# Kernel optimization log

Measured on AMD Instinct MI355X. Metric: run time of the kernel, lower is better.

## Reference

```python
import jax, jax.numpy as jnp
import numpy as np

SR = 16000; NFFT = 1024; HOP = 256; NMELS = 80; GRUH = 256; ZDIM = 16
NBINS = 65; HID = 512; B = 8; TLEN = 160000; PAD = NFFT // 2; IRLEN = 8000

def _consts():
    freqs = np.linspace(0, SR / 2, NFFT // 2 + 1); fsq = freqs ** 2
    aw = (12194.217 ** 2 * fsq ** 2) / ((fsq + 20.6 ** 2) * (fsq + 107.7 ** 2) * (fsq + 737.9 ** 2) * (fsq + 12194.217 ** 2) ** 0.5 + 1e-8)
    h2m = lambda f: 2595.0 * np.log10(1.0 + f / 700.0)
    m2h = lambda m: 700.0 * (10.0 ** (m / 2595.0) - 1.0)
    f_pts = m2h(np.linspace(h2m(0.0), h2m(SR / 2.0), NMELS + 2))
    fd = f_pts[1:] - f_pts[:-1]
    sl = f_pts[None, :] - freqs[:, None]
    fb = np.maximum(0.0, np.minimum(-sl[:, :-2] / fd[:-1], sl[:, 2:] / fd[1:]))
    win = 0.5 - 0.5 * np.cos(2.0 * np.pi * np.arange(NFFT) / NFFT)  # periodic hann
    return jnp.asarray(aw, jnp.float32), jnp.asarray(fb, jnp.float32), jnp.asarray(win, jnp.float32)
AW, MELFB, WIN = _consts()

def _frame(x, size, hop):
    n = (x.shape[-1] - size) // hop + 1
    idx = jnp.arange(n)[:, None] * hop + jnp.arange(size)[None, :]
    return x[:, idx]

def _stft(x):  # [B,T] -> [B, n_frames, 513] complex
    xp = jnp.pad(x, ((0, 0), (PAD, PAD)), mode='reflect')
    return jnp.fft.rfft(_frame(xp, NFFT, HOP) * WIN, axis=-1)

def _istft(spec, length):  # [B, n_frames, 513] -> [B, length]
    fr = jnp.fft.irfft(spec, n=NFFT, axis=-1) * WIN
    n = fr.shape[1]; total = (n - 1) * HOP + NFFT
    idx = (jnp.arange(n)[:, None] * HOP + jnp.arange(NFFT)[None, :]).reshape(-1)
    out = jnp.zeros((fr.shape[0], total), fr.dtype).at[:, idx].add(fr.reshape(fr.shape[0], -1))
    wsq = jnp.zeros((total,), WIN.dtype).at[idx].add(jnp.tile(WIN ** 2, (n,)))
    out = out / jnp.where(wsq > 1e-11, wsq, 1.0)
    return out[:, PAD:PAD + length]

def _lin_interp(x, size):  # torch F.interpolate(mode='linear', align_corners=False) on last axis
    L = x.shape[-1]
    pos = jnp.clip((jnp.arange(size) + 0.5) * (L / size) - 0.5, 0.0, L - 1.0)
    lo = jnp.floor(pos).astype(jnp.int32); hi = jnp.minimum(lo + 1, L - 1); w = pos - lo
    return x[..., lo] * (1.0 - w) + x[..., hi] * w

def _gru(x, wih, whh, bih, bhh):  # torch nn.GRU, batch_first, h0=0
    xp = x @ wih.T + bih
    def step(h, xt):
        gh = h @ whh.T + bhh
        xr, xz, xn = jnp.split(xt, 3, -1); hr, hz, hn = jnp.split(gh, 3, -1)
        r = jax.nn.sigmoid(xr + hr); z = jax.nn.sigmoid(xz + hz)
        nn_ = jnp.tanh(xn + r * hn)
        h = (1.0 - z) * nn_ + z * h
        return h, h
    h0 = jnp.zeros((x.shape[0], whh.shape[1]), x.dtype)
    _, hs = jax.lax.scan(step, h0, jnp.swapaxes(xp, 0, 1))
    return jnp.swapaxes(hs, 0, 1)

def _forward(audio, gender, age, gru_wih, gru_whh, gru_bih, gru_bhh, proj_w, proj_b,
             w0, b0, g0, e0, w1, b1, g1, e1, w2, b2, g2, e2,
             oq_w, oq_b, vt_w, vt_b, nf_w, nf_b, ir):
    # --- pitch via autocorrelation ---
    xp = jnp.pad(audio, ((0, 0), (PAD, PAD)), mode='reflect')
    fr = _frame(xp, NFFT, HOP)
    ps = jnp.abs(jnp.fft.rfft(fr, n=2 * NFFT, axis=-1)) ** 2
    ac = jnp.fft.irfft(ps, n=2 * NFFT, axis=-1)[..., :NFFT]
    ac = ac / (ac[..., :1] + 1e-8)
    min_lag, max_lag = SR // 1000, SR // 50  # 16, 320
    reg = ac[..., min_lag:max_lag]
    mv = jnp.max(reg, -1); mi = jnp.argmax(reg, -1)
    f0 = SR / (mi.astype(jnp.float32) + min_lag + 1e-8)
    f0 = jnp.where(mv < 0.3, 0.0, f0)[..., None]  # [B,F,1]
    # --- loudness + mels ---
    spec = jnp.abs(_stft(audio)) ** 2  # [B,F,513]
    loud = 10.0 * jnp.log10(jnp.mean((spec + 1e-8) * AW, -1, keepdims=True))  # [B,F,1]
    mels = jnp.log(spec @ MELFB + 1e-5)  # [B,F,80]
    mels = (mels - mels.mean(1, keepdims=True)) / jnp.sqrt(mels.var(1, keepdims=True) + 1e-5)
    z = _gru(mels, gru_wih, gru_whh, gru_bih, gru_bhh) @ proj_w.T + proj_b  # [B,F,16]
    Fn = f0.shape[1]
    # --- controller ---
    gb = jnp.broadcast_to(gender[:, None, :], (gender.shape[0], Fn, 2))
    ab = jnp.broadcast_to(age[:, None, :], (age.shape[0], Fn, 1))
    h = jnp.concatenate([z, (jnp.log(f0 + 1e-5) - 4.0) / 4.0, loud / 100.0 + 1.0, gb, ab], -1)
    for W, bb, gm, bt in ((w0, b0, g0, e0), (w1, b1, g1, e1), (w2, b2, g2, e2)):
        h = h @ W.T + bb
        h = (h - h.mean(-1, keepdims=True)) / jnp.sqrt(h.var(-1, keepdims=True) + 1e-5) * gm + bt
        h = jnp.where(h >= 0, h, 0.1 * h)  # LeakyReLU(0.1)
    oq = jax.nn.sigmoid(h @ oq_w.T + oq_b)
    vt = jax.nn.sigmoid(h @ vt_w.T + vt_b)
    nf = jax.nn.sigmoid(h @ nf_w.T + nf_b)
    amp = 10.0 ** (loud / 20.0)
    # --- decoder ---
    L = audio.shape[-1]
    f0u = _lin_interp(f0[..., 0], L); ampu = _lin_interp(amp[..., 0], L); oqu = _lin_interp(oq[..., 0], L)
    phase = jnp.cumsum(f0u / SR, -1); p = phase - jnp.floor(phase)
    oqc = jnp.clip(oqu, 0.1, 0.9)
    pulse = 0.5 * (1.0 - jnp.cos(jnp.pi * p / (oqc + 1e-8)))
    g = pulse * jax.nn.sigmoid((oqc - p) * 100.0)
    glottal = jnp.pad(g[..., 1:] - g[..., :-1], ((0, 0), (1, 0)))
    noise = jax.random.normal(jax.random.key(42), glottal.shape, glottal.dtype)
    def apply_filter(ex, filt):
        es = _stft(ex)  # [B,nf,513]
        ft = _lin_interp(jnp.swapaxes(filt, 1, 2), es.shape[1])  # time interp
        ff = _lin_interp(jnp.swapaxes(ft, 1, 2), es.shape[2])    # bin interp 65->513
        return _istft(es * ff, L)
    dry = (apply_filter(glottal, vt) + apply_filter(noise, nf)) * ampu
    # --- FFT reverb ---
    nconv = int(2 ** int(np.ceil(np.log2(L + IRLEN - 1))))
    wet = jnp.fft.irfft(jnp.fft.rfft(dry, n=nconv) * jnp.fft.rfft(ir, n=nconv), n=nconv)[..., :L]
    return wet, dry

def setup_inputs() -> dict:
    ks = iter(jax.random.split(jax.random.key(0), 48))
    def nrm(shape, s=0.05):
        return jax.random.normal(next(ks), shape, jnp.float32) * s
    inp = {}
    inp['audio'] = jax.random.normal(next(ks), (B, TLEN), jnp.float32)
    inp['gender'] = jax.random.uniform(next(ks), (B, 2), jnp.float32)
    inp['age'] = jax.random.uniform(next(ks), (B, 1), jnp.float32)
    inp['gru_wih'] = nrm((3 * GRUH, NMELS)); inp['gru_whh'] = nrm((3 * GRUH, GRUH))
    inp['gru_bih'] = jnp.zeros((3 * GRUH,), jnp.float32); inp['gru_bhh'] = jnp.zeros((3 * GRUH,), jnp.float32)
    inp['proj_w'] = nrm((ZDIM, GRUH)); inp['proj_b'] = jnp.zeros((ZDIM,), jnp.float32)
    din = ZDIM + 5
    inp['w0'] = nrm((HID, din)); inp['b0'] = jnp.zeros((HID,), jnp.float32)
    inp['g0'] = jnp.ones((HID,), jnp.float32); inp['e0'] = jnp.zeros((HID,), jnp.float32)
    inp['w1'] = nrm((HID, HID)); inp['b1'] = jnp.zeros((HID,), jnp.float32)
    inp['g1'] = jnp.ones((HID,), jnp.float32); inp['e1'] = jnp.zeros((HID,), jnp.float32)
    inp['w2'] = nrm((HID, HID)); inp['b2'] = jnp.zeros((HID,), jnp.float32)
    inp['g2'] = jnp.ones((HID,), jnp.float32); inp['e2'] = jnp.zeros((HID,), jnp.float32)
    inp['oq_w'] = nrm((1, HID)); inp['oq_b'] = jnp.zeros((1,), jnp.float32)
    inp['vt_w'] = nrm((NBINS, HID)); inp['vt_b'] = jnp.zeros((NBINS,), jnp.float32)
    inp['nf_w'] = nrm((NBINS, HID)); inp['nf_b'] = jnp.zeros((NBINS,), jnp.float32)
    decay = jnp.exp(-jnp.linspace(0.0, 5.0, IRLEN))
    inp['ir'] = jax.random.normal(next(ks), (IRLEN,), jnp.float32) * 0.1 * decay
    return inp

def reference(audio, gender, age, gru_wih, gru_whh, gru_bih, gru_bhh, proj_w, proj_b,
              w0, b0, g0, e0, w1, b1, g1, e1, w2, b2, g2, e2,
              oq_w, oq_b, vt_w, vt_b, nf_w, nf_b, ir):
    return _forward(audio, gender, age, gru_wih, gru_whh, gru_bih, gru_bhh, proj_w, proj_b,
                    w0, b0, g0, e0, w1, b1, g1, e1, w2, b2, g2, e2,
                    oq_w, oq_b, vt_w, vt_b, nf_w, nf_b, ir)
```

## Files before the change

### kernel.cpp

```cpp
#include <hip/hip_runtime.h>
#include <math.h>

#define SRF 16000.0f
#define HOP 256
#define FRM 626
#define BB 8
#define TLEN 160000
#define NFRM (BB*FRM)
#define NCONV 262144
#define ACCLEN 161024
#define GCH 40

constexpr size_t oWIN   = 0;
constexpr size_t oTW    = oWIN + 1024;
constexpr size_t oDIAG  = oTW + 1024;
constexpr size_t oTWF   = oDIAG + 16;
constexpr size_t oTWC   = oTWF + 1024;
constexpr size_t oAW    = oTWC + 1024;
constexpr size_t oMELFB = oAW + 513;
constexpr size_t oWSQI  = oMELFB + 513*80;
constexpr size_t oWIHT  = oWSQI + ACCLEN;
constexpr size_t oW0T   = oWIHT + 80*768;
constexpr size_t oW1T   = oW0T + 21*512;
constexpr size_t oW2T   = oW1T + 512*512;
constexpr size_t oVTT   = oW2T + 512*512;
constexpr size_t oNFT   = oVTT + 512*65;
constexpr size_t oF0    = oNFT + 512*65;
constexpr size_t oLOUD  = oF0 + NFRM;
constexpr size_t oOQ    = oLOUD + NFRM;
constexpr size_t oVT    = oOQ + NFRM;
constexpr size_t oNF    = oVT + (size_t)NFRM*65;
constexpr size_t oGLOT  = oNF + (size_t)NFRM*65;
constexpr size_t oNOISE = oGLOT + (size_t)BB*TLEN;
constexpr size_t oACC   = oNOISE + (size_t)BB*TLEN;
constexpr size_t oCONVA = oACC + (size_t)BB*ACCLEN;
constexpr size_t oEND   = oCONVA + (size_t)9*NCONV*2;
constexpr size_t oXP    = oEND;
constexpr size_t oGSUM  = oXP + (size_t)NFRM*768;
constexpr size_t oGPRE  = oGSUM + 320;
constexpr size_t oEND2  = oGPRE + 640;
constexpr size_t oCONVB = oWSQI;
constexpr size_t oMEL = oCONVA;
constexpr size_t oHS  = oMEL + (size_t)NFRM*80;

constexpr long R_WIN=1024, R_TW=512, R_TWF=512, R_TWC=512, R_AW=513, R_MELFB=41040,
  R_WSQI=161024, R_WIHT=61440, R_W0T=10752, R_W1T=262144, R_W2T=262144,
  R_VTT=33280, R_NFT=33280, R_IR=NCONV;
constexpr long INIT_TOTAL = R_WIN+R_TW+R_TWF+R_TWC+R_AW+R_MELFB+R_WSQI+R_WIHT+R_W0T+
  R_W1T+R_W2T+R_VTT+R_NFT+R_IR;

constexpr int NOISEB = 313;
constexpr int ZACCB  = 315;
constexpr int MEGA_BLOCKS = 1 + NFRM + NOISEB + ZACCB;

typedef float f32x4 __attribute__((ext_vector_type(4)));
typedef __bf16 bf16x8 __attribute__((ext_vector_type(8)));
typedef short short8 __attribute__((ext_vector_type(8)));
#define MFMA_BF16 __builtin_amdgcn_mfma_f32_16x16x32_bf16

__device__ inline int mirror_idx(int j) {
  if (j < 0) j = -j;
  if (j >= TLEN) j = 2*TLEN - 2 - j;
  return j;
}
__device__ inline float sigm(float x) { return 1.0f/(1.0f + expf(-x)); }
__device__ inline unsigned short f2bf(float x) {
  unsigned u = __float_as_uint(x);
  return (unsigned short)((u + 0x7FFFu + ((u >> 16) & 1u)) >> 16);
}
__device__ inline float tanh_fast(float x) {
  return 1.0f - 2.0f/(__expf(2.0f*x) + 1.0f);
}

__device__ inline float interpF(const float* v, int i) {
  float pos = ((float)i + 0.5f) * (626.0f/160000.0f) - 0.5f;
  pos = fminf(fmaxf(pos, 0.0f), 625.0f);
  int lo = (int)floorf(pos);
  int hi = min(lo + 1, 625);
  float w = pos - (float)lo;
  return v[lo]*(1.0f - w) + v[hi]*w;
}
__device__ inline float interp65(const float* v, int k) {
  float pos = ((float)k + 0.5f) * (65.0f/513.0f) - 0.5f;
  pos = fminf(fmaxf(pos, 0.0f), 64.0f);
  int lo = (int)floorf(pos);
  int hi = min(lo + 1, 64);
  float w = pos - (float)lo;
  return v[lo]*(1.0f - w) + v[hi]*w;
}
__device__ inline float gwave(float ph, float oqu) {
  float p = ph - floorf(ph);
  float oqc = fminf(fmaxf(oqu, 0.1f), 0.9f);
  float pulse = 0.5f*(1.0f - cosf(3.14159265358979f * p / (oqc + 1e-8f)));
  float gs = 1.0f/(1.0f + __expf(-(oqc - p)*100.0f));
  return pulse*gs;
}

template<int LOGN, int TS>
__device__ inline void fft2(float2* c, const float2* tw, int tid, int nthr, bool inv) {
  constexpr int N = 1 << LOGN;
  for (int s = 1; s <= LOGN; ++s) {
    const int half = 1 << (s-1);
    const int tstep = (N >> s) * TS;
    for (int bf = tid; bf < (N>>1); bf += nthr) {
      int jj = bf & (half-1);
      int i0 = ((bf >> (s-1)) << s) + jj;
      int i1 = i0 + half;
      float2 wv = tw[jj*tstep];
      float wi = inv ? -wv.y : wv.y;
      float2 u = c[i0], v = c[i1];
      float tr  = v.x*wv.x - v.y*wi;
      float tci = v.x*wi  + v.y*wv.x;
      c[i0] = make_float2(u.x + tr, u.y + tci);
      c[i1] = make_float2(u.x - tr, u.y - tci);
    }
    __syncthreads();
  }
}

__device__ inline void threefry2x32(unsigned k0, unsigned k1, unsigned x0, unsigned x1,
                                    unsigned& o0, unsigned& o1) {
  unsigned ks2 = k0 ^ k1 ^ 0x1BD11BDAu;
  x0 += k0; x1 += k1;
#define TF_R(r) { x0 += x1; x1 = (x1<<(r)) | (x1>>(32-(r))); x1 ^= x0; }
  TF_R(13) TF_R(15) TF_R(26) TF_R(6)
  x0 += k1; x1 += ks2 + 1u;
  TF_R(17) TF_R(29) TF_R(16) TF_R(24)
  x0 += ks2; x1 += k0 + 2u;
  TF_R(13) TF_R(15) TF_R(26) TF_R(6)
  x0 += k0; x1 += k1 + 3u;
  TF_R(17) TF_R(29) TF_R(16) TF_R(24)
  x0 += k1; x1 += ks2 + 4u;
  TF_R(13) TF_R(15) TF_R(26) TF_R(6)
  x0 += ks2; x1 += k0 + 5u;
#undef TF_R
  o0 = x0; o1 = x1;
}

__device__ inline float erfinv_f(float x) {
  float w = -log1pf(-x*x);
  float p;
  if (w < 5.0f) {
    w = w - 2.5f;
    p = 2.81022636e-08f;
    p = fmaf(p, w, 3.43273939e-07f);
    p = fmaf(p, w, -3.5233877e-06f);
    p = fmaf(p, w, -4.39150654e-06f);
    p = fmaf(p, w, 0.00021858087f);
    p = fmaf(p, w, -0.00125372503f);
    p = fmaf(p, w, -0.00417768164f);
    p = fmaf(p, w, 0.246640727f);
    p = fmaf(p, w, 1.50140941f);
  } else {
    w = sqrtf(w) - 3.0f;
    p = -0.000200214257f;
    p = fmaf(p, w, 0.000100950558f);
    p = fmaf(p, w, 0.00134934322f);
    p = fmaf(p, w, -0.00367342844f);
    p = fmaf(p, w, 0.00573950773f);
    p = fmaf(p, w, -0.0076224613f);
    p = fmaf(p, w, 0.00943887047f);
    p = fmaf(p, w, 1.00167406f);
    p = fmaf(p, w, 2.83297682f);
  }
  return p*x;
}
__device__ inline float normal_from_bits(unsigned bits) {
  float f = __uint_as_float((bits >> 9) | 0x3F800000u) - 1.0f;
  float x = fmaxf(-0.99999994f, fmaf(f, 1.99999994f, -0.99999994f));
  return 1.41421356237f * erfinv_f(x);
}

__device__ inline double mel_fpt(int j) {
  double mmax = 2595.0 * log10(1.0 + 8000.0/700.0);
  return 700.0 * (pow(10.0, (mmax * (double)j / 81.0) / 2595.0) - 1.0);
}

__global__ void k_init(float* W, const float* wih, const float* w0,
                       const float* w1, const float* w2, const float* vtw, const float* nfw,
                       const float* ir) {
  long id = (long)blockIdx.x*256 + threadIdx.x;
  if (id < R_WIN) {
    double w = 0.5 - 0.5*cos(2.0*M_PI*(double)id/1024.0);
    W[oWIN+id] = (float)w; return;
  } id -= R_WIN;
  if (id < R_TW) {
    double a = -2.0*M_PI*(double)id/1024.0;
    W[oTW+2*id] = (float)cos(a); W[oTW+2*id+1] = (float)sin(a); return;
  } id -= R_TW;
  if (id < R_TWF) {
    double a = -2.0*M_PI*(double)id/262144.0;
    W[oTWF+2*id] = (float)cos(a); W[oTWF+2*id+1] = (float)sin(a); return;
  } id -= R_TWF;
  if (id < R_TWC) {
    double a = -2.0*M_PI*(double)id/512.0;
    W[oTWC+2*id] = (float)cos(a); W[oTWC+2*id+1] = (float)sin(a); return;
  } id -= R_TWC;
  if (id < R_AW) {
    double fr = (double)id*(8000.0/512.0); double fsq = fr*fr;
    double num = 12194.217*12194.217*fsq*fsq;
    double den = (fsq+20.6*20.6)*(fsq+107.7*107.7)*(fsq+737.9*737.9)*sqrt(fsq+12194.217*12194.217) + 1e-8;
    W[oAW+id] = (float)(num/den); return;
  } id -= R_AW;
  if (id < R_MELFB) {
    int k = (int)(id/80), m = (int)(id%80);
    double fk = (double)k*(8000.0/512.0);
    double f0p = mel_fpt(m), f1p = mel_fpt(m+1), f2p = mel_fpt(m+2);
    double lower = (fk - f0p)/(f1p - f0p);
    double upper = (f2p - fk)/(f2p - f1p);
    double v = fmax(0.0, fmin(lower, upper));
    W[oMELFB+id] = (float)v; return;
  } id -= R_MELFB;
  if (id < R_WSQI) {
    int t = (int)id;
    int n1 = t/256; if (n1 > 625) n1 = 625;
    int n0t = t - 1023 + 255; int n0 = (n0t > 0) ? n0t/256 : 0;
    double s = 0.0;
    for (int n = n0; n <= n1; ++n) {
      int o = t - n*256;
      double wv = 0.5 - 0.5*cos(2.0*M_PI*(double)o/1024.0);
      s += wv*wv;
    }
    float sf = (float)s;
    W[oWSQI+t] = (sf > 1e-11f) ? (1.0f/sf) : 1.0f; return;
  } id -= R_WSQI;
  if (id < R_WIHT) { long k = id/768, g = id%768; W[oWIHT+id] = wih[g*80+k];  return; } id -= R_WIHT;
  if (id < R_W0T)  { long d = id/512, j = id%512; W[oW0T+id] = w0[j*21+d];   return; } id -= R_W0T;
  if (id < R_W1T)  { long k = id/512, j = id%512; W[oW1T+id] = w1[j*512+k];  return; } id -= R_W1T;
  if (id < R_W2T)  { long k = id/512, j = id%512; W[oW2T+id] = w2[j*512+k];  return; } id -= R_W2T;
  if (id < R_VTT)  { long k = id/65,  m = id%65;  W[oVTT+id] = vtw[m*512+k]; return; } id -= R_VTT;
  if (id < R_NFT)  { long k = id/65,  m = id%65;  W[oNFT+id] = nfw[m*512+k]; return; } id -= R_NFT;
  if (id < R_IR) {
    size_t base = oCONVA + 2*((size_t)8*NCONV + id);
    W[base] = (id < 8000) ? ir[id] : 0.0f; W[base+1] = 0.0f; return;
  }
}

__global__ __launch_bounds__(256) void k_stft_mel(const float* audio, float* W) {
  int blk = blockIdx.x; int b = blk/FRM, f = blk%FRM; int tid = threadIdx.x;
  __shared__ float2 cb[1024];
  __shared__ float spec[513];
  __shared__ float redbuf[4];
  const float* arow = audio + (size_t)b*TLEN;
  const float2* tw = (const float2*)(W + oTW);
  for (int i = tid; i < 1024; i += 256) {
    float v = arow[mirror_idx(f*256 + i - 512)] * W[oWIN + i];
    int pos = __brev((unsigned)i) >> 22;
    cb[pos] = make_float2(v, 0.f);
  }
  __syncthreads();
  fft2<10,1>(cb, tw, tid, 256, false);
  for (int k = tid; k < 513; k += 256) { float2 z = cb[k]; spec[k] = z.x*z.x + z.y*z.y; }
  __syncthreads();
  float part = 0.f;
  for (int k = tid; k < 513; k += 256) part += (spec[k] + 1e-8f) * W[oAW + k];
  for (int off = 32; off; off >>= 1) part += __shfl_down(part, off, 64);
  if ((tid & 63) == 0) redbuf[tid >> 6] = part;
  __syncthreads();
  if (tid == 0) {
    float s = redbuf[0]+redbuf[1]+redbuf[2]+redbuf[3];
    W[oLOUD + blk] = 10.0f * log10f(s / 513.0f);
  }
  for (int m = tid; m < 80; m += 256) {
    double f0p = mel_fpt(m), f2p = mel_fpt(m + 2);
    int klo = (int)(f0p * (512.0/8000.0)); if (klo < 0) klo = 0;
    int khi = (int)(f2p * (512.0/8000.0)) + 1; if (khi > 512) khi = 512;
    float s = 0.f;
    for (int k = klo; k <= khi; ++k) s += spec[k]*W[oMELFB + (size_t)k*80 + m];
    W[oMEL + (size_t)blk*80 + m] = logf(s + 1e-5f);
  }
}

__global__ void k_melnorm(float* W) {
  int id = blockIdx.x*256 + threadIdx.x;
  if (id >= BB*80) return;
  int b = id/80, m = id%80;
  double s = 0.0, ss = 0.0;
  for (int f = 0; f < FRM; ++f) {
    double v = W[oMEL + ((size_t)b*FRM + f)*80 + m];
    s += v; ss += v*v;
  }
  double mean = s/FRM;
  double var = ss/FRM - mean*mean;
  float mu = (float)mean;
  float rstd = (float)(1.0/sqrt(var + 1e-5));
  for (int f = 0; f < FRM; ++f) {
    size_t idx = oMEL + ((size_t)b*FRM + f)*80 + m;
    W[idx] = (W[idx] - mu)*rstd;
  }
}

__global__ void k_xp(float* W, const float* bih) {
  size_t id = (size_t)blockIdx.x*256 + threadIdx.x;
  if (id >= (size_t)NFRM*768) return;
  int g = (int)(id % 768);
  size_t q = id / 768;
  const float* mrow = W + oMEL + q*80;
  float acc = bih[g];
  for (int k = 0; k < 80; ++k) acc = fmaf(mrow[k], W[oWIHT + (size_t)k*768 + g], acc);
  W[oXP + q*768 + g] = acc;
}

__global__ __launch_bounds__(512, 2) void k_mega(float* W, const float* audio,
                                                 const float* whh, const float* bhh) {
  __shared__ unsigned short sB[32768];
  __shared__ unsigned short sA[4096];
  __shared__ float sGT[9216];
  __shared__ float fr4[4][1032];
  __shared__ float wpow[8];
  __shared__ float wmax[8];
  __shared__ int   wmaxi[8];
  int tid = threadIdx.x;
  int blk = blockIdx.x;

  if (blk == 0) {
    int w = tid >> 6, l = tid & 63;
    const float* XP = W + oXP;
    float* HS = W + oHS;

    for (int idx = tid; idx < 32768; idx += 512) {
      int lcol = idx >> 8, k = idx & 255;
      int gcol = 96*(lcol >> 4) + 80 + (lcol & 15);
      sB[lcol*256 + (k ^ ((lcol & 7) << 3))] = f2bf(whh[(size_t)gcol*256 + k]);
    }
    for (int idx = tid; idx < 4096; idx += 512) sA[idx] = 0;

    int cl = l & 15, khalf = (l >> 4) * 8;
    bf16x8 bw[40];
    #pragma unroll
    for (int t2 = 0; t2 < 5; ++t2) {
      int col = 96*w + 16*t2 + cl;
      #pragma unroll
      for (int kk = 0; kk < 8; ++kk) {
        const float* src = whh + (size_t)col*256 + kk*32 + khalf;
        short8 tmp;
        #pragma unroll
        for (int j = 0; j < 8; ++j) tmp[j] = (short)f2bf(src[j]);
        bw[t2*8 + kk] = __builtin_bit_cast(bf16x8, tmp);
      }
    }

    int g = tid & 255, bbase = tid >> 8;
    float bh_r = bhh[g], bh_z = bhh[256 + g], bh_n = bhh[512 + g];
    float hprev[4] = {0.f, 0.f, 0.f, 0.f};
    int aXor = (cl & 7) << 3;
    int lcol5 = w*16 + cl;
    int rowg = l >> 4;
    int colb = 96*w + cl;
    int gtw = colb*12 + rowg*4;
    int gtr0 = g*12 + 4*bbase;
    int gtr1 = (256 + g)*12 + 4*bbase;
    int gtr2 = (512 + g)*12 + 4*bbase;

    __syncthreads();

#define LDA(kk) (*(const bf16x8*)&sA[(cl)*256 + (((kk)*32 + khalf) ^ aXor)])
#define LDB(kk) (*(const bf16x8*)&sB[(lcol5)*256 + (((kk)*32 + khalf) ^ aXor)])
#define STEPK(A_, kk) \
      c0 = MFMA_BF16(A_, bw[0*8+(kk)], c0, 0, 0, 0); \
      c1 = MFMA_BF16(A_, bw[1*8+(kk)], c1, 0, 0, 0); \
      c2 = MFMA_BF16(A_, bw[2*8+(kk)], c2, 0, 0, 0); \
      c3 = MFMA_BF16(A_, bw[3*8+(kk)], c3, 0, 0, 0); \
      c4 = MFMA_BF16(A_, bw[4*8+(kk)], c4, 0, 0, 0); \
      c5 = MFMA_BF16(A_, LDB(kk), c5, 0, 0, 0);

    for (int t = 0; t < FRM; ++t) {
      float xr[4], xz[4], xn[4];
      #pragma unroll
      for (int j = 0; j < 4; ++j) {
        const float* xpp = XP + ((size_t)(4*bbase + j)*FRM + t)*768 + g;
        xr[j] = xpp[0]; xz[j] = xpp[256]; xn[j] = xpp[512];
      }
      f32x4 c0 = {0,0,0,0}, c1 = {0,0,0,0}, c2 = {0,0,0,0};
      f32x4 c3 = {0,0,0,0}, c4 = {0,0,0,0}, c5 = {0,0,0,0};
      bf16x8 a0 = LDA(0), a1 = LDA(1), a2 = LDA(2), a3 = LDA(3);
      STEPK(a0, 0) STEPK(a1, 1) STEPK(a2, 2) STEPK(a3, 3)
      a0 = LDA(4); a1 = LDA(5); a2 = LDA(6); a3 = LDA(7);
      STEPK(a0, 4) STEPK(a1, 5) STEPK(a2, 6) STEPK(a3, 7)
      if (rowg < 3) {
        *(f32x4*)&sGT[gtw + 0*192]  = c0;
        *(f32x4*)&sGT[gtw + 1*192]  = c1;
        *(f32x4*)&sGT[gtw + 2*192]  = c2;
        *(f32x4*)&sGT[gtw + 3*192]  = c3;
        *(f32x4*)&sGT[gtw + 4*192]  = c4;
        *(f32x4*)&sGT[gtw + 5*192]  = c5;
      }
      __syncthreads();
      f32x4 rv = *(const f32x4*)&sGT[gtr0];
      f32x4 zv = *(const f32x4*)&sGT[gtr1];
      f32x4 nv = *(const f32x4*)&sGT[gtr2];
      #pragma unroll
      for (int j = 0; j < 4; ++j) {
        int bb = 4*bbase + j;
        float r = 1.0f/(1.0f + __expf(-(xr[j] + rv[j] + bh_r)));
        float z = 1.0f/(1.0f + __expf(-(xz[j] + zv[j] + bh_z)));
        float nn = tanh_fast(xn[j] + r*(nv[j] + bh_n));
        float h = (1.0f - z)*nn + z*hprev[j];
        hprev[j] = h;
        HS[((size_t)bb*FRM + t)*256 + g] = h;
        sA[bb*256 + (g ^ ((bb & 7) << 3))] = f2bf(h);
      }
      __syncthreads();
    }
#undef LDA
#undef LDB
#undef STEPK
    return;
  }
  blk -= 1;

  if (blk < NFRM) {
    int b = blk/FRM, f = blk%FRM;
    const float* arow = audio + (size_t)b*TLEN;
    for (int idx = tid; idx < 4*1032; idx += 512) {
      int s = idx/1032, i = idx - s*1032;
      int j = i + s;
      fr4[s][i] = (j < 1024) ? arow[mirror_idx(f*256 + j - 512)] : 0.f;
    }
    __syncthreads();
    int lane = tid & 63, wv = tid >> 6;
    float p = 0.f;
    for (int i = tid; i < 1024; i += 512) { float x = fr4[0][i]; p += x*x; }
    for (int off = 32; off; off >>= 1) p += __shfl_down(p, off, 64);
    if (lane == 0) wpow[wv] = p;
    float vbest = -1e30f; int ibest = tid;
    if (tid < 304) {
      int lag = 16 + tid;
      int s = lag & 3, base = lag - s;
      int qmax = (1023 - lag) >> 2;
      float acc = 0.f;
      for (int q = 0; q <= qmax; ++q) {
        float4 u = *(const float4*)&fr4[0][4*q];
        float4 v = *(const float4*)&fr4[s][base + 4*q];
        acc += u.x*v.x + u.y*v.y + u.z*v.z + u.w*v.w;
      }
      vbest = acc;
    }
    for (int off = 32; off; off >>= 1) {
      float v2 = __shfl_down(vbest, off, 64);
      int i2 = __shfl_down(ibest, off, 64);
      if (v2 > vbest || (v2 == vbest && i2 < ibest)) { vbest = v2; ibest = i2; }
    }
    if (lane == 0) { wmax[wv] = vbest; wmaxi[wv] = ibest; }
    __syncthreads();
    if (tid == 0) {
      float ac0 = 0.f;
      #pragma unroll
      for (int q = 0; q < 8; ++q) ac0 += wpow[q];
      float bv = wmax[0]; int bi = wmaxi[0];
      #pragma unroll
      for (int q = 1; q < 8; ++q) {
        if (wmax[q] > bv || (wmax[q] == bv && wmaxi[q] < bi)) { bv = wmax[q]; bi = wmaxi[q]; }
      }
      float inv = 1.0f/(ac0 + 1e-8f);
      float best = bv*inv;
      W[oF0 + (size_t)blk] = (best < 0.3f) ? 0.0f : (SRF/(float)(bi + 16));
    }
    return;
  }
  blk -= NFRM;

  if (blk < NOISEB) {
    size_t base = (size_t)blk*4096;
    #pragma unroll
    for (int j = 0; j < 8; ++j) {
      size_t p = base + (size_t)j*512 + tid;
      if (p < (size_t)BB*TLEN) {
        unsigned o0, o1;
        threefry2x32(0u, 42u, 0u, (unsigned)p, o0, o1);
        W[oNOISE + p] = normal_from_bits(o0 ^ o1);
      }
    }
    return;
  }
  blk -= NOISEB;

  {
    size_t base = (size_t)blk*4096;
    #pragma unroll
    for (int j = 0; j < 8; ++j) {
      size_t p = base + (size_t)j*512 + tid;
      if (p < (size_t)BB*ACCLEN) W[oACC + p] = 0.0f;
    }
  }
}

__device__ inline void ln_lrelu(float acc[8], float gj, float ej, float out[8][512],
                                float wred[8][8][2], float stat[8][2],
                                int tid, int lane, int wv, int j) {
  #pragma unroll
  for (int i = 0; i < 8; ++i) {
    float s = acc[i], ss = acc[i]*acc[i];
    for (int off = 32; off; off >>= 1) { s += __shfl_down(s, off, 64); ss += __shfl_down(ss, off, 64); }
    if (lane == 0) { wred[i][wv][0] = s; wred[i][wv][1] = ss; }
  }
  __syncthreads();
  if (tid < 8) {
    float s = 0.f, ss = 0.f;
    #pragma unroll
    for (int w = 0; w < 8; ++w) { s += wred[tid][w][0]; ss += wred[tid][w][1]; }
    float mean = s/512.0f;
    float var = ss/512.0f - mean*mean;
    stat[tid][0] = mean;
    stat[tid][1] = 1.0f/sqrtf(var + 1e-5f);
  }
  __syncthreads();
  #pragma unroll
  for (int i = 0; i < 8; ++i) {
    float v = (acc[i] - stat[i][0])*stat[i][1]*gj + ej;
    out[i][j] = (v >= 0.f) ? v : 0.1f*v;
  }
}

__global__ __launch_bounds__(512) void k_mlp(float* W, const float* gender, const float* age,
    const float* projw, const float* projb,
    const float* b0, const float* g0, const float* e0,
    const float* b1, const float* g1, const float* e1,
    const float* b2, const float* g2, const float* e2,
    const float* oqw, const float* oqb, const float* vtb, const float* nfb) {
  __shared__ float hbuf[8][256];
  __shared__ float in0[8][21];
  __shared__ float actA[8][512];
  __shared__ float actB[8][512];
  __shared__ float wred[8][8][2];
  __shared__ float stat[8][2];
  int tid = threadIdx.x; int q0 = blockIdx.x*8;
  for (int x = tid; x < 2048; x += 512) {
    int i = x >> 8, k = x & 255;
    hbuf[i][k] = W[oHS + ((size_t)(q0 + i))*256 + k];
  }
  __syncthreads();
  if (tid < 128) {
    int i = tid >> 4, zi = tid & 15;
    float a = projb[zi];
    for (int k = 0; k < 256; ++k) a = fmaf(hbuf[i][k], projw[zi*256 + k], a);
    in0[i][zi] = a;
  } else if (tid < 168) {
    int x = tid - 128; int i = x/5, d = 16 + x%5;
    int q = q0 + i; int b = q/FRM;
    float v;
    if (d == 16) v = (logf(W[oF0 + q] + 1e-5f) - 4.0f)*0.25f;
    else if (d == 17) v = W[oLOUD + q]/100.0f + 1.0f;
    else if (d == 18) v = gender[b*2];
    else if (d == 19) v = gender[b*2 + 1];
    else v = age[b];
    in0[i][d] = v;
  }
  __syncthreads();
  int j = tid, lane = tid & 63, wv = tid >> 6;
  float acc[8];
  #pragma unroll
  for (int i = 0; i < 8; ++i) acc[i] = b0[j];
  for (int d = 0; d < 21; ++d) {
    float w = W[oW0T + (size_t)d*512 + j];
    #pragma unroll
    for (int i = 0; i < 8; ++i) acc[i] = fmaf(in0[i][d], w, acc[i]);
  }
  ln_lrelu(acc, g0[j], e0[j], actA, wred, stat, tid, lane, wv, j);
  __syncthreads();
  #pragma unroll
  for (int i = 0; i < 8; ++i) acc[i] = b1[j];
  for (int k = 0; k < 512; ++k) {
    float w = W[oW1T + (size_t)k*512 + j];
    #pragma unroll
    for (int i = 0; i < 8; ++i) acc[i] = fmaf(actA[i][k], w, acc[i]);
  }
  ln_lrelu(acc, g1[j], e1[j], actB, wred, stat, tid, lane, wv, j);
  __syncthreads();
  #pragma unroll
  for (int i = 0; i < 8; ++i) acc[i] = b2[j];
  for (int k = 0; k < 512; ++k) {
    float w = W[oW2T + (size_t)k*512 + j];
    #pragma unroll
    for (int i = 0; i < 8; ++i) acc[i] = fmaf(actB[i][k], w, acc[i]);
  }
  ln_lrelu(acc, g2[j], e2[j], actA, wred, stat, tid, lane, wv, j);
  __syncthreads();
  for (int x = tid; x < 520; x += 512) {
    int i = x/65, m = x%65;
    float a = vtb[m], a2 = nfb[m];
    for (int k = 0; k < 512; ++k) {
      float h = actA[i][k];
      a  = fmaf(h, W[oVTT + (size_t)k*65 + m], a);
      a2 = fmaf(h, W[oNFT + (size_t)k*65 + m], a2);
    }
    W[oVT + (size_t)(q0+i)*65 + m] = sigm(a);
    W[oNF + (size_t)(q0+i)*65 + m] = sigm(a2);
  }
  if (tid < 8) {
    float a = oqb[0];
    for (int k = 0; k < 512; ++k) a = fmaf(actA[tid][k], oqw[k], a);
    W[oOQ + q0 + tid] = sigm(a);
  }
}

__global__ __launch_bounds__(256) void k_gsum(float* W) {
  int blk = blockIdx.x; int b = blk/GCH, c = blk%GCH; int tid = threadIdx.x;
  __shared__ float ws[4];
  const float* f0r = W + oF0 + (size_t)b*FRM;
  int i0 = c*4096 + tid*16;
  float s = 0.f;
  #pragma unroll
  for (int j = 0; j < 16; ++j) {
    int i = i0 + j;
    if (i < TLEN) s += interpF(f0r, i)*(1.0f/SRF);
  }
  for (int off = 32; off; off >>= 1) s += __shfl_down(s, off, 64);
  if ((tid & 63) == 0) ws[tid >> 6] = s;
  __syncthreads();
  if (tid == 0) W[oGSUM + (size_t)b*GCH + c] = ws[0]+ws[1]+ws[2]+ws[3];
}

__global__ void k_gscan(float* W) {
  if (blockIdx.x == 0 && threadIdx.x == 0) {
    double* P = (double*)(W + oGPRE);
    for (int b = 0; b < BB; ++b) {
      double a = 0.0;
      for (int c = 0; c < GCH; ++c) {
        P[b*GCH + c] = a;
        a += (double)W[oGSUM + (size_t)b*GCH + c];
      }
    }
  }
}

__global__ __launch_bounds__(256) void k_gapply(float* W) {
  int blk = blockIdx.x; int b = blk/GCH, c = blk%GCH; int tid = threadIdx.x;
  __shared__ float wss[4];
  __shared__ float lastw[4];
  const float* f0r = W + oF0 + (size_t)b*FRM;
  const float* oqr = W + oOQ + (size_t)b*FRM;
  float* grow = W + oGLOT + (size_t)b*TLEN;
  double P = ((const double*)(W + oGPRE))[b*GCH + c];
  int i0 = c*4096 + tid*16;
  int lane = tid & 63, wv = tid >> 6;
  float v[16]; float ts = 0.f;
  #pragma unroll
  for (int j = 0; j < 16; ++j) {
    int i = i0 + j;
    float x = (i < TLEN) ? interpF(f0r, i)*(1.0f/SRF) : 0.f;
    v[j] = x; ts += x;
  }
  float sc = ts;
  #pragma unroll
  for (int off = 1; off < 64; off <<= 1) {
    float o = __shfl_up(sc, off, 64);
    if (lane >= off) sc += o;
  }
  if (lane == 63) wss[wv] = sc;
  __syncthreads();
  float wpre = 0.f;
  for (int q = 0; q < wv; ++q) wpre += wss[q];
  double ph0 = P + (double)(wpre + sc - ts);
  float run = 0.f; float gq[16];
  #pragma unroll
  for (int j = 0; j < 16; ++j) {
    int i = i0 + j;
    run += v[j];
    float ph = (float)(ph0 + (double)run);
    gq[j] = gwave(ph, interpF(oqr, min(i, TLEN-1)));
  }
  float prev = __shfl_up(gq[15], 1, 64);
  if (lane == 63) lastw[wv] = gq[15];
  __syncthreads();
  if (lane == 0) {
    if (wv > 0) prev = lastw[wv - 1];
    else if (i0 > 0) prev = gwave((float)P, interpF(oqr, i0 - 1));
    else prev = 0.f;
  }
  #pragma unroll
  for (int j = 0; j < 16; ++j) {
    int i = i0 + j;
    if (i < TLEN) {
      float gl = (j == 0) ? prev : gq[j-1];
      grow[i] = (i == 0) ? 0.f : (gq[j] - gl);
    }
  }
}

__global__ __launch_bounds__(256) void k_filtsynth(float* W) {
  int blk = blockIdx.x; int b = blk/FRM, f = blk%FRM; int tid = threadIdx.x;
  __shared__ float2 cG[1024], cN[1024];
  __shared__ float fvt[65], fnf[65];
  const float* grow = W + oGLOT + (size_t)b*TLEN;
  const float* nrow = W + oNOISE + (size_t)b*TLEN;
  const float2* tw = (const float2*)(W + oTW);
  for (int i = tid; i < 1024; i += 256) {
    int si = mirror_idx(f*256 + i - 512);
    float wv = W[oWIN + i];
    int pos = __brev((unsigned)i) >> 22;
    cG[pos] = make_float2(grow[si]*wv, 0.f);
    cN[pos] = make_float2(nrow[si]*wv, 0.f);
  }
  if (tid < 65) {
    fvt[tid] = W[oVT + ((size_t)b*FRM + f)*65 + tid];
    fnf[tid] = W[oNF + ((size_t)b*FRM + f)*65 + tid];
  }
  __syncthreads();
  fft2<10,1>(cG, tw, tid, 256, false);
  fft2<10,1>(cN, tw, tid, 256, false);
  for (int k = tid; k < 1024; k += 256) {
    int kp = min(k, 1024 - k);
    float fv = interp65(fvt, kp);
    float fn = interp65(fnf, kp);
    float2 zg = cG[k], zn = cN[k];
    cG[k] = make_float2(zg.x*fv + zn.x*fn, zg.y*fv + zn.y*fn);
  }
  __syncthreads();
  for (int i = tid; i < 1024; i += 256) {
    int jj = __brev((unsigned)i) >> 22;
    if (jj > i) { float2 t2 = cG[i]; cG[i] = cG[jj]; cG[jj] = t2; }
  }
  __syncthreads();
  fft2<10,1>(cG, tw, tid, 256, true);
  float* arow = W + oACC + (size_t)b*ACCLEN + (size_t)f*256;
  for (int i = tid; i < 1024; i += 256) {
    float xv = cG[i].x*(1.0f/1024.0f)*W[oWIN + i];
    atomicAdd(arow + i, xv);
  }
}

__global__ void k_dry(float* W, float* dout) {
  size_t id = (size_t)blockIdx.x*256 + threadIdx.x;
  if (id >= (size_t)BB*NCONV) return;
  int b = (int)(id / NCONV);
  int n = (int)(id % NCONV);
  float dv = 0.f;
  if (n < TLEN) {
    float val = W[oACC + (size_t)b*ACCLEN + 512 + n] * W[oWSQI + 512 + n];
    const float* lrow = W + oLOUD + (size_t)b*FRM;
    float pos = ((float)n + 0.5f) * (626.0f/160000.0f) - 0.5f;
    pos = fminf(fmaxf(pos, 0.0f), 625.0f);
    int lo = (int)floorf(pos);
    int hi = min(lo + 1, 625);
    float w = pos - (float)lo;
    float a0 = exp10f(lrow[lo]*0.05f);
    float a1 = exp10f(lrow[hi]*0.05f);
    float ampu = a0*(1.0f - w) + a1*w;
    dv = val*ampu;
    dout[(size_t)BB*TLEN + (size_t)b*TLEN + n] = dv;
  }
  ((float2*)(W + oCONVA))[id] = make_float2(dv, 0.f);
}

__global__ __launch_bounds__(256) void k_conv_f1(const float* in, float* out,
                                                 const float* tw, const float* twf,
                                                 const float* twc) {
  int blk = blockIdx.x; int t = blk >> 9; int bcol = blk & 511; int tid = threadIdx.x;
  __shared__ float2 cb[512];
  const float2* src = (const float2*)in + (size_t)t*NCONV;
  for (int a = tid; a < 512; a += 256) {
    int pos = __brev((unsigned)a) >> 23;
    cb[pos] = src[(size_t)a*512 + bcol];
  }
  __syncthreads();
  fft2<9,2>(cb, (const float2*)tw, tid, 256, false);
  float2* dst = (float2*)out + (size_t)t*NCONV + (size_t)bcol*512;
  for (int k1 = tid; k1 < 512; k1 += 256) {
    unsigned m = (unsigned)bcol * (unsigned)k1;
    float2 tc = ((const float2*)twc)[m >> 9];
    float2 tf = ((const float2*)twf)[m & 511];
    float wr = tc.x*tf.x - tc.y*tf.y;
    float wi = tc.x*tf.y + tc.y*tf.x;
    float2 v = cb[k1];
    dst[k1] = make_float2(v.x*wr - v.y*wi, v.x*wi + v.y*wr);
  }
}

__global__ __launch_bounds__(256) void k_conv_f2(const float* in, float* out, const float* tw) {
  int blk = blockIdx.x; int t = blk >> 9; int k1 = blk & 511; int tid = threadIdx.x;
  __shared__ float2 cb[512];
  const float2* src = (const float2*)in + (size_t)t*NCONV;
  for (int bb2 = tid; bb2 < 512; bb2 += 256) {
    int pos = __brev((unsigned)bb2) >> 23;
    cb[pos] = src[(size_t)bb2*512 + k1];
  }
  __syncthreads();
  fft2<9,2>(cb, (const float2*)tw, tid, 256, false);
  float2* dst = (float2*)out + (size_t)t*NCONV;
  for (int k2 = tid; k2 < 512; k2 += 256) {
    dst[(size_t)k1 + 512*(size_t)k2] = cb[k2];
  }
}

__global__ void k_mul(float* W) {
  size_t id = (size_t)blockIdx.x*256 + threadIdx.x;
  if (id >= (size_t)BB*NCONV) return;
  size_t k = id % NCONV;
  float2* A = (float2*)(W + oCONVA);
  float2 a = A[id];
  float2 c = A[(size_t)8*NCONV + k];
  float pr = a.x*c.x - a.y*c.y;
  float pi = a.x*c.y + a.y*c.x;
  A[id] = make_float2(pr, -pi);
}

__global__ void k_wet(const float* W, float* dout) {
  size_t id = (size_t)blockIdx.x*256 + threadIdx.x;
  if (id >= (size_t)BB*TLEN) return;
  size_t b = id / TLEN, n = id % TLEN;
  dout[id] = ((const float2*)(W + oCONVA))[b*NCONV + n].x * (1.0f/262144.0f);
}

extern "C" void kernel_launch(void* const* d_in, const int* in_sizes, int n_in,
                              void* d_out, int out_size, void* d_ws, size_t ws_size,
                              hipStream_t stream) {
  (void)in_sizes; (void)n_in; (void)out_size; (void)ws_size;
  const float* audio  = (const float*)d_in[0];
  const float* gender = (const float*)d_in[1];
  const float* age    = (const float*)d_in[2];
  const float* wih    = (const float*)d_in[3];
  const float* whh    = (const float*)d_in[4];
  const float* bih    = (const float*)d_in[5];
  const float* bhh    = (const float*)d_in[6];
  const float* projw  = (const float*)d_in[7];
  const float* projb  = (const float*)d_in[8];
  const float* w0     = (const float*)d_in[9];
  const float* b0     = (const float*)d_in[10];
  const float* g0     = (const float*)d_in[11];
  const float* e0     = (const float*)d_in[12];
  const float* w1     = (const float*)d_in[13];
  const float* b1     = (const float*)d_in[14];
  const float* g1     = (const float*)d_in[15];
  const float* e1     = (const float*)d_in[16];
  const float* w2     = (const float*)d_in[17];
  const float* b2     = (const float*)d_in[18];
  const float* g2     = (const float*)d_in[19];
  const float* e2     = (const float*)d_in[20];
  const float* oqw    = (const float*)d_in[21];
  const float* oqb    = (const float*)d_in[22];
  const float* vtw    = (const float*)d_in[23];
  const float* vtb    = (const float*)d_in[24];
  const float* nfw    = (const float*)d_in[25];
  const float* nfb    = (const float*)d_in[26];
  const float* ir     = (const float*)d_in[27];
  float* W = (float*)d_ws;
  float* dout = (float*)d_out;

  k_init<<<(int)((INIT_TOTAL + 255)/256), 256, 0, stream>>>(W, wih, w0, w1, w2, vtw, nfw, ir);
  k_stft_mel<<<NFRM, 256, 0, stream>>>(audio, W);
  k_melnorm<<<3, 256, 0, stream>>>(W);
  k_xp<<<(int)(((size_t)NFRM*768 + 255)/256), 256, 0, stream>>>(W, bih);
  k_mega<<<MEGA_BLOCKS, 512, 0, stream>>>(W, audio, whh, bhh);
  k_mlp<<<NFRM/8, 512, 0, stream>>>(W, gender, age, projw, projb,
                                    b0, g0, e0, b1, g1, e1, b2, g2, e2, oqw, oqb, vtb, nfb);
  k_gsum<<<BB*GCH, 256, 0, stream>>>(W);
  k_gscan<<<1, 64, 0, stream>>>(W);
  k_gapply<<<BB*GCH, 256, 0, stream>>>(W);
  k_filtsynth<<<NFRM, 256, 0, stream>>>(W);
  k_dry<<<(int)(((size_t)BB*NCONV + 255)/256), 256, 0, stream>>>(W, dout);
  k_conv_f1<<<9*512, 256, 0, stream>>>(W + oCONVA, W + oCONVB, W + oTW, W + oTWF, W + oTWC);
  k_conv_f2<<<9*512, 256, 0, stream>>>(W + oCONVB, W + oCONVA, W + oTW);
  k_mul<<<(int)(((size_t)BB*NCONV + 255)/256), 256, 0, stream>>>(W);
  k_conv_f1<<<8*512, 256, 0, stream>>>(W + oCONVA, W + oCONVB, W + oTW, W + oTWF, W + oTWC);
  k_conv_f2<<<8*512, 256, 0, stream>>>(W + oCONVB, W + oCONVA, W + oTW);
  k_wet<<<(int)(((size_t)BB*TLEN + 255)/256), 256, 0, stream>>>(W, dout);
}
```

Measured before the change: 2.229 ms.

## Pack real signals into complex FFTs for filter synthesis and convolution

```diff
diff --git a/kernel.cpp b/kernel.cpp
--- a/kernel.cpp
+++ b/kernel.cpp
@@ -34,7 +34,7 @@
 constexpr size_t oNOISE = oGLOT + (size_t)BB*TLEN;
 constexpr size_t oACC   = oNOISE + (size_t)BB*TLEN;
 constexpr size_t oCONVA = oACC + (size_t)BB*ACCLEN;
-constexpr size_t oEND   = oCONVA + (size_t)9*NCONV*2;
+constexpr size_t oEND   = oCONVA + (size_t)5*NCONV*2;
 constexpr size_t oXP    = oEND;
 constexpr size_t oGSUM  = oXP + (size_t)NFRM*768;
 constexpr size_t oGPRE  = oGSUM + 320;
@@ -231,7 +231,7 @@
   if (id < R_VTT)  { long k = id/65,  m = id%65;  W[oVTT+id] = vtw[m*512+k]; return; } id -= R_VTT;
   if (id < R_NFT)  { long k = id/65,  m = id%65;  W[oNFT+id] = nfw[m*512+k]; return; } id -= R_NFT;
   if (id < R_IR) {
-    size_t base = oCONVA + 2*((size_t)8*NCONV + id);
+    size_t base = oCONVA + 2*((size_t)4*NCONV + id);
     W[base] = (id < 8000) ? ir[id] : 0.0f; W[base+1] = 0.0f; return;
   }
 }
@@ -304,7 +304,7 @@
 __global__ __launch_bounds__(512, 2) void k_mega(float* W, const float* audio,
                                                  const float* whh, const float* bhh) {
   __shared__ unsigned short sB[32768];
-  __shared__ unsigned short sA[4096];
+  __shared__ unsigned short sA[2048];
   __shared__ float sGT[9216];
   __shared__ float fr4[4][1032];
   __shared__ float wpow[8];
@@ -323,7 +323,7 @@
       int gcol = 96*(lcol >> 4) + 80 + (lcol & 15);
       sB[lcol*256 + (k ^ ((lcol & 7) << 3))] = f2bf(whh[(size_t)gcol*256 + k]);
     }
-    for (int idx = tid; idx < 4096; idx += 512) sA[idx] = 0;
+    for (int idx = tid; idx < 2048; idx += 512) sA[idx] = 0;
 
     int cl = l & 15, khalf = (l >> 4) * 8;
     bf16x8 bw[40];
@@ -339,6 +339,8 @@
         bw[t2*8 + kk] = __builtin_bit_cast(bf16x8, tmp);
       }
     }
+    const short8 zzs = {0,0,0,0,0,0,0,0};
+    const bf16x8 z8 = __builtin_bit_cast(bf16x8, zzs);
 
     int g = tid & 255, bbase = tid >> 8;
     float bh_r = bhh[g], bh_z = bhh[256 + g], bh_n = bhh[512 + g];
@@ -351,6 +353,7 @@
     int gtr0 = g*12 + 4*bbase;
     int gtr1 = (256 + g)*12 + 4*bbase;
     int gtr2 = (512 + g)*12 + 4*bbase;
+    bool aOK = (cl < 8);
 
     __syncthreads();
 
@@ -373,9 +376,10 @@
       }
       f32x4 c0 = {0,0,0,0}, c1 = {0,0,0,0}, c2 = {0,0,0,0};
       f32x4 c3 = {0,0,0,0}, c4 = {0,0,0,0}, c5 = {0,0,0,0};
-      bf16x8 a0 = LDA(0), a1 = LDA(1), a2 = LDA(2), a3 = LDA(3);
+      bf16x8 a0 = z8, a1 = z8, a2 = z8, a3 = z8;
+      if (aOK) { a0 = LDA(0); a1 = LDA(1); a2 = LDA(2); a3 = LDA(3); }
       STEPK(a0, 0) STEPK(a1, 1) STEPK(a2, 2) STEPK(a3, 3)
-      a0 = LDA(4); a1 = LDA(5); a2 = LDA(6); a3 = LDA(7);
+      if (aOK) { a0 = LDA(4); a1 = LDA(5); a2 = LDA(6); a3 = LDA(7); }
       STEPK(a0, 4) STEPK(a1, 5) STEPK(a2, 6) STEPK(a3, 7)
       if (rowg < 3) {
         *(f32x4*)&sGT[gtw + 0*192]  = c0;
@@ -680,7 +684,7 @@
 
 __global__ __launch_bounds__(256) void k_filtsynth(float* W) {
   int blk = blockIdx.x; int b = blk/FRM, f = blk%FRM; int tid = threadIdx.x;
-  __shared__ float2 cG[1024], cN[1024];
+  __shared__ float2 cZ[1024], cS[1024];
   __shared__ float fvt[65], fnf[65];
   const float* grow = W + oGLOT + (size_t)b*TLEN;
   const float* nrow = W + oNOISE + (size_t)b*TLEN;
@@ -689,58 +693,59 @@
     int si = mirror_idx(f*256 + i - 512);
     float wv = W[oWIN + i];
     int pos = __brev((unsigned)i) >> 22;
-    cG[pos] = make_float2(grow[si]*wv, 0.f);
-    cN[pos] = make_float2(nrow[si]*wv, 0.f);
+    cZ[pos] = make_float2(grow[si]*wv, nrow[si]*wv);
   }
   if (tid < 65) {
     fvt[tid] = W[oVT + ((size_t)b*FRM + f)*65 + tid];
     fnf[tid] = W[oNF + ((size_t)b*FRM + f)*65 + tid];
   }
   __syncthreads();
-  fft2<10,1>(cG, tw, tid, 256, false);
-  fft2<10,1>(cN, tw, tid, 256, false);
-  for (int k = tid; k < 1024; k += 256) {
-    int kp = min(k, 1024 - k);
-    float fv = interp65(fvt, kp);
-    float fn = interp65(fnf, kp);
-    float2 zg = cG[k], zn = cN[k];
-    cG[k] = make_float2(zg.x*fv + zn.x*fn, zg.y*fv + zn.y*fn);
-  }
-  __syncthreads();
-  for (int i = tid; i < 1024; i += 256) {
-    int jj = __brev((unsigned)i) >> 22;
-    if (jj > i) { float2 t2 = cG[i]; cG[i] = cG[jj]; cG[jj] = t2; }
-  }
-  __syncthreads();
-  fft2<10,1>(cG, tw, tid, 256, true);
+  fft2<10,1>(cZ, tw, tid, 256, false);
+  for (int k = tid; k <= 512; k += 256) {
+    int km = (1024 - k) & 1023;
+    float2 z1 = cZ[k], z2 = cZ[km];
+    float Gr = 0.5f*(z1.x + z2.x), Gi = 0.5f*(z1.y - z2.y);
+    float Nr = 0.5f*(z1.y + z2.y), Ni = 0.5f*(z2.x - z1.x);
+    float fv = interp65(fvt, k), fn = interp65(fnf, k);
+    float Sr = Gr*fv + Nr*fn, Si = Gi*fv + Ni*fn;
+    cS[__brev((unsigned)k) >> 22] = make_float2(Sr, Si);
+    if (km != k) cS[__brev((unsigned)km) >> 22] = make_float2(Sr, -Si);
+  }
+  __syncthreads();
+  fft2<10,1>(cS, tw, tid, 256, true);
   float* arow = W + oACC + (size_t)b*ACCLEN + (size_t)f*256;
   for (int i = tid; i < 1024; i += 256) {
-    float xv = cG[i].x*(1.0f/1024.0f)*W[oWIN + i];
+    float xv = cS[i].x*(1.0f/1024.0f)*W[oWIN + i];
     atomicAdd(arow + i, xv);
   }
 }
 
 __global__ void k_dry(float* W, float* dout) {
   size_t id = (size_t)blockIdx.x*256 + threadIdx.x;
-  if (id >= (size_t)BB*NCONV) return;
-  int b = (int)(id / NCONV);
+  if (id >= (size_t)4*NCONV) return;
+  int t = (int)(id / NCONV);
   int n = (int)(id % NCONV);
-  float dv = 0.f;
+  float dv0 = 0.f, dv1 = 0.f;
   if (n < TLEN) {
-    float val = W[oACC + (size_t)b*ACCLEN + 512 + n] * W[oWSQI + 512 + n];
-    const float* lrow = W + oLOUD + (size_t)b*FRM;
     float pos = ((float)n + 0.5f) * (626.0f/160000.0f) - 0.5f;
     pos = fminf(fmaxf(pos, 0.0f), 625.0f);
     int lo = (int)floorf(pos);
     int hi = min(lo + 1, 625);
-    float w = pos - (float)lo;
-    float a0 = exp10f(lrow[lo]*0.05f);
-    float a1 = exp10f(lrow[hi]*0.05f);
-    float ampu = a0*(1.0f - w) + a1*w;
-    dv = val*ampu;
-    dout[(size_t)BB*TLEN + (size_t)b*TLEN + n] = dv;
-  }
-  ((float2*)(W + oCONVA))[id] = make_float2(dv, 0.f);
+    float wgt = pos - (float)lo;
+    float wsq = W[oWSQI + 512 + n];
+    #pragma unroll
+    for (int q = 0; q < 2; ++q) {
+      int b = 2*t + q;
+      float val = W[oACC + (size_t)b*ACCLEN + 512 + n] * wsq;
+      const float* lrow = W + oLOUD + (size_t)b*FRM;
+      float a0 = exp10f(lrow[lo]*0.05f);
+      float a1 = exp10f(lrow[hi]*0.05f);
+      float dv = val*(a0*(1.0f - wgt) + a1*wgt);
+      if (q == 0) dv0 = dv; else dv1 = dv;
+      dout[(size_t)BB*TLEN + (size_t)b*TLEN + n] = dv;
+    }
+  }
+  ((float2*)(W + oCONVA))[id] = make_float2(dv0, dv1);
 }
 
 __global__ __launch_bounds__(256) void k_conv_f1(const float* in, float* out,
@@ -784,22 +789,33 @@
 }
 
 __global__ void k_mul(float* W) {
+  constexpr size_t HALF = NCONV/2;
   size_t id = (size_t)blockIdx.x*256 + threadIdx.x;
-  if (id >= (size_t)BB*NCONV) return;
-  size_t k = id % NCONV;
+  if (id >= (size_t)4*(HALF + 1)) return;
+  int t = (int)(id / (HALF + 1));
+  size_t k = id % (HALF + 1);
+  size_t km = (NCONV - k) & (NCONV - 1);
   float2* A = (float2*)(W + oCONVA);
-  float2 a = A[id];
-  float2 c = A[(size_t)8*NCONV + k];
-  float pr = a.x*c.x - a.y*c.y;
-  float pi = a.x*c.y + a.y*c.x;
-  A[id] = make_float2(pr, -pi);
+  float2 z1 = A[(size_t)t*NCONV + k];
+  float2 z2 = A[(size_t)t*NCONV + km];
+  float2 c  = A[(size_t)4*NCONV + k];
+  float X0r = 0.5f*(z1.x + z2.x), X0i = 0.5f*(z1.y - z2.y);
+  float X1r = 0.5f*(z1.y + z2.y), X1i = 0.5f*(z2.x - z1.x);
+  float P0r = X0r*c.x - X0i*c.y, P0i = X0r*c.y + X0i*c.x;
+  float P1r = X1r*c.x - X1i*c.y, P1i = X1r*c.y + X1i*c.x;
+  A[(size_t)t*NCONV + k] = make_float2(P0r - P1i, -(P0i + P1r));
+  if (km != k) {
+    A[(size_t)t*NCONV + km] = make_float2(P0r + P1i, P0i - P1r);
+  }
 }
 
 __global__ void k_wet(const float* W, float* dout) {
   size_t id = (size_t)blockIdx.x*256 + threadIdx.x;
   if (id >= (size_t)BB*TLEN) return;
   size_t b = id / TLEN, n = id % TLEN;
-  dout[id] = ((const float2*)(W + oCONVA))[b*NCONV + n].x * (1.0f/262144.0f);
+  float2 V = ((const float2*)(W + oCONVA))[(b >> 1)*NCONV + n];
+  float val = (b & 1) ? -V.y : V.x;
+  dout[id] = val * (1.0f/262144.0f);
 }
 
 extern "C" void kernel_launch(void* const* d_in, const int* in_sizes, int n_in,
@@ -848,11 +864,11 @@
   k_gscan<<<1, 64, 0, stream>>>(W);
   k_gapply<<<BB*GCH, 256, 0, stream>>>(W);
   k_filtsynth<<<NFRM, 256, 0, stream>>>(W);
-  k_dry<<<(int)(((size_t)BB*NCONV + 255)/256), 256, 0, stream>>>(W, dout);
-  k_conv_f1<<<9*512, 256, 0, stream>>>(W + oCONVA, W + oCONVB, W + oTW, W + oTWF, W + oTWC);
-  k_conv_f2<<<9*512, 256, 0, stream>>>(W + oCONVB, W + oCONVA, W + oTW);
-  k_mul<<<(int)(((size_t)BB*NCONV + 255)/256), 256, 0, stream>>>(W);
-  k_conv_f1<<<8*512, 256, 0, stream>>>(W + oCONVA, W + oCONVB, W + oTW, W + oTWF, W + oTWC);
-  k_conv_f2<<<8*512, 256, 0, stream>>>(W + oCONVB, W + oCONVA, W + oTW);
+  k_dry<<<(int)(((size_t)4*NCONV + 255)/256), 256, 0, stream>>>(W, dout);
+  k_conv_f1<<<5*512, 256, 0, stream>>>(W + oCONVA, W + oCONVB, W + oTW, W + oTWF, W + oTWC);
+  k_conv_f2<<<5*512, 256, 0, stream>>>(W + oCONVB, W + oCONVA, W + oTW);
+  k_mul<<<(int)(((size_t)4*(NCONV/2 + 1) + 255)/256), 256, 0, stream>>>(W);
+  k_conv_f1<<<4*512, 256, 0, stream>>>(W + oCONVA, W + oCONVB, W + oTW, W + oTWF, W + oTWC);
+  k_conv_f2<<<4*512, 256, 0, stream>>>(W + oCONVB, W + oCONVA, W + oTW);
   k_wet<<<(int)(((size_t)BB*TLEN + 255)/256), 256, 0, stream>>>(W, dout);
 }
```

New measurement: 2.199 ms. Within noise of the previous version (-1.4%).
